# Kernel optimization log

Measured on AMD Instinct MI355X. Metric: run time of the kernel, lower is better.

The kernel has to match this reference:

```python
import math
import jax, jax.numpy as jnp
import numpy as np

ORDER = 3      # polynomial order of latent motion
N = 512        # numOfNodes
D = 4          # dim
B = 4          # number of (tInit, tLast, eventTimes) tuples in `data`
S = 10         # numOfSamples (quadrature points per interval)
E = 20         # events per interval


def setup_inputs() -> dict:
    key = jax.random.key(0)
    k1, k2, k3 = jax.random.split(key, 3)
    gamma = jax.random.uniform(k1, (N,), dtype=jnp.float32)          # torch.rand(N,1) squeezed
    z0 = jax.random.normal(k2, (ORDER, N, D), dtype=jnp.float32)     # stacked z0[o]
    t_init = jnp.arange(B, dtype=jnp.float32)                        # interval starts
    t_last = t_init + 1.0                                            # interval ends (tInit < tLast)
    event_times = t_init[:, None] + jax.random.uniform(k3, (B, E), dtype=jnp.float32)
    ii, jj = np.triu_indices(N, k=1)                                 # torch.triu_indices(N, N, offset=1)
    pair_i = jnp.asarray(ii, dtype=jnp.int32)
    pair_j = jnp.asarray(jj, dtype=jnp.int32)
    return {"gamma": gamma, "z0": z0, "t_init": t_init, "t_last": t_last,
            "event_times": event_times, "pair_i": pair_i, "pair_j": pair_j}


def _positions(z0, t):
    # z(i, t) = sum_o z0[o, i] * t^o / o!   ; t: [T] -> returns [T, N, D]
    O = z0.shape[0]
    fact = jnp.asarray([math.factorial(o) for o in range(O)], dtype=z0.dtype)
    pw = (t[:, None] ** jnp.arange(O, dtype=z0.dtype)) / fact        # [T, O]
    return jnp.einsum('to,ond->tnd', pw, z0)


def _log_intensity(gamma, z0, pair_i, pair_j, t):
    # log lambda_ij(t) = gamma_i + gamma_j - ||z_i(t) - z_j(t)||_2 ; t: [T] -> [T, P]
    z = _positions(z0, t)                                            # [T, N, D]
    diff = z[:, pair_i, :] - z[:, pair_j, :]                         # [T, P, D]
    dist = jnp.sqrt(jnp.sum(diff * diff, axis=-1))                   # [T, P]
    return gamma[pair_i][None, :] + gamma[pair_j][None, :] - dist


def reference(gamma, z0, t_init, t_last, event_times, pair_i, pair_j):
    # Riemann-sum integral: linspace(tInit, tLast, S, endpoint=False) with step (tLast-tInit)/S
    step = (t_last - t_init) / S                                     # [B]
    tq = t_init[:, None] + step[:, None] * jnp.arange(S, dtype=t_init.dtype)[None, :]  # [B, S]
    log_lam_q = _log_intensity(gamma, z0, pair_i, pair_j, tq.reshape(-1))              # [B*S, P]
    integral = jnp.sum(jnp.exp(log_lam_q).reshape(B, S, -1) * step[:, None, None])
    # sum of log intensities at all event times, over all node pairs
    log_lam_e = _log_intensity(gamma, z0, pair_i, pair_j, event_times.reshape(-1))     # [B*E, P]
    neg_log_likelihood = integral - jnp.sum(log_lam_e)
    return neg_log_likelihood
```

## Files before the change

kernel.cpp:

```cpp
#include <hip/hip_runtime.h>
#include <hip/hip_fp16.h>
#include <math.h>

#define TPB 512
#define NCHUNK 8

#if __has_builtin(__builtin_amdgcn_exp2f)
#define EXP2(x) __builtin_amdgcn_exp2f(x)
#else
#define EXP2(x) exp2f(x)
#endif


template <bool QUAD>
__device__ __forceinline__ float pair_loop(
    int tid, int N, int d0, int dfull, bool hasHalf,
    const float2* zsh, const float* egsh, __half2 zi01, __half2 zi23)
{
    const int mask = N - 1;
    float acc = 0.0f;
    #pragma unroll 4
    for (int dd = d0; dd < dfull; ++dd) {
        int j = (tid + dd) & mask;
        float2 p = zsh[j];
        __half2 zj01 = *reinterpret_cast<const __half2*>(&p.x);
        __half2 zj23 = *reinterpret_cast<const __half2*>(&p.y);
        __half2 d01 = __hsub2(zi01, zj01);
        __half2 d23 = __hsub2(zi23, zj23);
        __half2 hq  = __hfma2(d23, d23, __hmul2(d01, d01));
        float q = __half2float(__hadd(__low2half(hq), __high2half(hq)));
        float dist = __builtin_amdgcn_sqrtf(q);
        if (QUAD) acc += egsh[j] * EXP2(-dist);
        else      acc += dist;
    }
    if (hasHalf && tid < (N >> 1)) {
        int j = (tid + (N >> 1)) & mask;
        float2 p = zsh[j];
        __half2 zj01 = *reinterpret_cast<const __half2*>(&p.x);
        __half2 zj23 = *reinterpret_cast<const __half2*>(&p.y);
        __half2 d01 = __hsub2(zi01, zj01);
        __half2 d23 = __hsub2(zi23, zj23);
        __half2 hq  = __hfma2(d23, d23, __hmul2(d01, d01));
        float q = __half2float(__hadd(__low2half(hq), __high2half(hq)));
        float dist = __builtin_amdgcn_sqrtf(q);
        if (QUAD) acc += egsh[j] * EXP2(-dist);
        else      acc += dist;
    }
    return acc;
}

__global__ __launch_bounds__(TPB) void nhpp_partial(
    const float* __restrict__ gamma,
    const float* __restrict__ z0,
    const float* __restrict__ t_init,
    const float* __restrict__ t_last,
    const float* __restrict__ event_times,
    float*       __restrict__ partials,
    int N, int B, int S, int E)
{
    __shared__ float2 zsh[TPB];
    __shared__ float  egsh[TPB];
    __shared__ double wsum[TPB / 64];

    const int tid = threadIdx.x;
    const int tt  = blockIdx.y;
    const int BS  = B * S;

    float t, w;
    bool quad;
    if (tt < BS) {
        int b = tt / S, s = tt - b * S;
        float ti = t_init[b];
        float st = (t_last[b] - ti) / (float)S;
        t = ti + st * (float)s;
        w = st;
        quad = true;
    } else {
        int idx = tt - BS;
        int b = idx / E, e = idx - b * E;
        t = event_times[b * E + e];
        w = 1.0f;
        quad = false;
    }

    const float c1 = t;
    const float c2 = 0.5f * t * t;
    const float sc = quad ? 1.4426950408889634f : 1.0f;
    const float4* z0v = (const float4*)z0;
    __half2 zi01 = __floats2half2_rn(0.f, 0.f);
    __half2 zi23 = zi01;
    float gi = 0.f;
    if (tid < N) {
        float4 a0 = z0v[tid];
        float4 a1 = z0v[N + tid];
        float4 a2 = z0v[2 * N + tid];
        float zx = (a0.x + c1 * a1.x + c2 * a2.x) * sc;
        float zy = (a0.y + c1 * a1.y + c2 * a2.y) * sc;
        float zz = (a0.z + c1 * a1.z + c2 * a2.z) * sc;
        float zw = (a0.w + c1 * a1.w + c2 * a2.w) * sc;
        zi01 = __floats2half2_rn(zx, zy);
        zi23 = __floats2half2_rn(zz, zw);
        float2 packed;
        packed.x = *reinterpret_cast<float*>(&zi01);
        packed.y = *reinterpret_cast<float*>(&zi23);
        zsh[tid] = packed;
        gi = gamma[tid];
        if (quad) egsh[tid] = __expf(gi);
    }
    __syncthreads();

    const int dpc = (N / 2) / NCHUNK;
    const int d0  = 1 + dpc * blockIdx.x;
    const int d1  = 1 + dpc * (blockIdx.x + 1);
    const bool hasHalf = (d1 == N / 2 + 1);
    const int dfull = hasHalf ? d1 - 1 : d1;

    float acc = 0.0f;
    if (tid < N) {
        if (quad) {
            acc = pair_loop<true >(tid, N, d0, dfull, hasHalf, zsh, egsh, zi01, zi23);
            acc *= w * __expf(gi);
        } else {
            acc = pair_loop<false>(tid, N, d0, dfull, hasHalf, zsh, egsh, zi01, zi23);
            acc -= gi * (float)(2 * (dfull - d0) + (hasHalf ? 1 : 0));
        }
    }

    for (int off = 32; off > 0; off >>= 1)
        acc += __shfl_down(acc, off, 64);
    if ((tid & 63) == 0) wsum[tid >> 6] = (double)acc;
    __syncthreads();
    if (tid == 0) {
        double s = 0.0;
        #pragma unroll
        for (int k = 0; k < TPB / 64; ++k) s += wsum[k];
        partials[tt * NCHUNK + blockIdx.x] = (float)s;
    }
}

__global__ __launch_bounds__(256) void nhpp_reduce(
    const float4* __restrict__ partials4, int n4, float* __restrict__ out)
{
    __shared__ double wsum[256 / 64];
    double acc = 0.0;
    for (int k = threadIdx.x; k < n4; k += 256) {
        float4 v = partials4[k];
        acc += (double)v.x + (double)v.y + (double)v.z + (double)v.w;
    }
    for (int off = 32; off > 0; off >>= 1)
        acc += __shfl_down(acc, off, 64);
    if ((threadIdx.x & 63) == 0) wsum[threadIdx.x >> 6] = acc;
    __syncthreads();
    if (threadIdx.x == 0) {
        double s = 0.0;
        #pragma unroll
        for (int k = 0; k < 4; ++k) s += wsum[k];
        out[0] = (float)s;
    }
}

extern "C" void kernel_launch(void* const* d_in, const int* in_sizes, int n_in,
                              void* d_out, int out_size, void* d_ws, size_t ws_size,
                              hipStream_t stream)
{
    const float* gamma   = (const float*)d_in[0];
    const float* z0      = (const float*)d_in[1];
    const float* t_init  = (const float*)d_in[2];
    const float* t_last  = (const float*)d_in[3];
    const float* ev      = (const float*)d_in[4];

    const int N = in_sizes[0];
    const int B = in_sizes[2];
    const int E = in_sizes[4] / B;
    const int S = 10;
    const int T = B * S + B * E;

    float* partials = (float*)d_ws;

    dim3 grid(NCHUNK, T);
    nhpp_partial<<<grid, TPB, 0, stream>>>(gamma, z0, t_init, t_last, ev,
                                           partials, N, B, S, E);
    nhpp_reduce<<<1, 256, 0, stream>>>((const float4*)partials, (T * NCHUNK) / 4,
                                       (float*)d_out);
}
```

Before: 15.56 us.

## Fuse final reduction into main kernel via atomics and halve chunk count

Replaces the second reduction kernel with a double-precision atomicAdd accumulator plus a last-block-done counter, so the final sum is written by the last finishing block. A memset of the accumulator and counter is added before the launch. NCHUNK also drops from 8 to 4, giving fewer blocks that each do more pair work. The aim is to remove a kernel launch and its dependency gap. In exchange it adds a memset node, atomic contention on a single address, and a nondeterministic summation order.

```diff
diff --git a/kernel.cpp b/kernel.cpp
--- a/kernel.cpp
+++ b/kernel.cpp
@@ -3,7 +3,7 @@
 #include <math.h>
 
 #define TPB 512
-#define NCHUNK 8
+#define NCHUNK 4
 
 #if __has_builtin(__builtin_amdgcn_exp2f)
 #define EXP2(x) __builtin_amdgcn_exp2f(x)
@@ -49,13 +49,15 @@
     return acc;
 }
 
-__global__ __launch_bounds__(TPB) void nhpp_partial(
+__global__ __launch_bounds__(TPB) void nhpp_fused(
     const float* __restrict__ gamma,
     const float* __restrict__ z0,
     const float* __restrict__ t_init,
     const float* __restrict__ t_last,
     const float* __restrict__ event_times,
-    float*       __restrict__ partials,
+    double*      __restrict__ acc_ptr,
+    unsigned*    __restrict__ cnt_ptr,
+    float*       __restrict__ out,
     int N, int B, int S, int E)
 {
     __shared__ float2 zsh[TPB];
@@ -134,28 +136,14 @@
         double s = 0.0;
         #pragma unroll
         for (int k = 0; k < TPB / 64; ++k) s += wsum[k];
-        partials[tt * NCHUNK + blockIdx.x] = (float)s;
-    }
-}
-
-__global__ __launch_bounds__(256) void nhpp_reduce(
-    const float4* __restrict__ partials4, int n4, float* __restrict__ out)
-{
-    __shared__ double wsum[256 / 64];
-    double acc = 0.0;
-    for (int k = threadIdx.x; k < n4; k += 256) {
-        float4 v = partials4[k];
-        acc += (double)v.x + (double)v.y + (double)v.z + (double)v.w;
-    }
-    for (int off = 32; off > 0; off >>= 1)
-        acc += __shfl_down(acc, off, 64);
-    if ((threadIdx.x & 63) == 0) wsum[threadIdx.x >> 6] = acc;
-    __syncthreads();
-    if (threadIdx.x == 0) {
-        double s = 0.0;
-        #pragma unroll
-        for (int k = 0; k < 4; ++k) s += wsum[k];
-        out[0] = (float)s;
+        atomicAdd(acc_ptr, s);
+        __threadfence();
+        unsigned old = atomicAdd(cnt_ptr, 1u);
+        if (old == (unsigned)(gridDim.x * gridDim.y) - 1u) {
+            __threadfence();
+            double tot = atomicAdd(acc_ptr, 0.0);
+            out[0] = (float)tot;
+        }
     }
 }
 
@@ -175,11 +163,12 @@
     const int S = 10;
     const int T = B * S + B * E;
 
-    float* partials = (float*)d_ws;
+    double*   acc = (double*)d_ws;
+    unsigned* cnt = (unsigned*)((char*)d_ws + 8);
+
+    hipMemsetAsync(d_ws, 0, 16, stream);
 
     dim3 grid(NCHUNK, T);
-    nhpp_partial<<<grid, TPB, 0, stream>>>(gamma, z0, t_init, t_last, ev,
-                                           partials, N, B, S, E);
-    nhpp_reduce<<<1, 256, 0, stream>>>((const float4*)partials, (T * NCHUNK) / 4,
-                                       (float*)d_out);
+    nhpp_fused<<<grid, TPB, 0, stream>>>(gamma, z0, t_init, t_last, ev,
+                                         acc, cnt, (float*)d_out, N, B, S, E);
 }
```

New measurement: 26.97 us. +73.3%, slower.
